# Kernel optimization log

Hardware: AMD Instinct MI355X
Metric: run time of the kernel (lower is better)

Reference implementation:

```python
import jax, jax.numpy as jnp
import numpy as np

D = 1024      # embedding_dim
H = 16        # n_heads
HD = D // H   # head_dim
EPS = 1e-05


def layernorm(x, scale, bias):
    # torch.var default is unbiased (ddof=1) in the original module
    mean = jnp.mean(x, axis=-1, keepdims=True)
    var = jnp.var(x, axis=-1, keepdims=True, ddof=1)
    return scale * (x - mean) / jnp.sqrt(var + EPS) + bias


def gelu(x):
    return 0.5 * x * (1 + jnp.tanh(0.79788456 * (x + 0.044715 * x ** 3)))


def setup_inputs() -> dict:
    key = jax.random.key(0)
    ks = jax.random.split(key, 12)
    s = 0.02
    return {
        "x": jax.random.normal(ks[0], (2, 2048, D), dtype=jnp.float32),
        "Wq": jax.random.normal(ks[1], (D, D), dtype=jnp.float32) * s,
        "Wk": jax.random.normal(ks[2], (D, D), dtype=jnp.float32) * s,
        "Wv": jax.random.normal(ks[3], (D, D), dtype=jnp.float32) * s,
        "Wo": jax.random.normal(ks[4], (D, D), dtype=jnp.float32) * s,
        "bo": jnp.zeros((D,), dtype=jnp.float32),
        "W1": jax.random.normal(ks[5], (D, 4 * D), dtype=jnp.float32) * s,
        "b1": jnp.zeros((4 * D,), dtype=jnp.float32),
        "W2": jax.random.normal(ks[6], (4 * D, D), dtype=jnp.float32) * s,
        "b2": jnp.zeros((D,), dtype=jnp.float32),
        "ln1_scale": jnp.ones((D,), dtype=jnp.float32),
        "ln1_bias": jnp.zeros((D,), dtype=jnp.float32),
        "ln2_scale": jnp.ones((D,), dtype=jnp.float32),
        "ln2_bias": jnp.zeros((D,), dtype=jnp.float32),
    }


def reference(x, Wq, Wk, Wv, Wo, bo, W1, b1, W2, b2,
              ln1_scale, ln1_bias, ln2_scale, ln2_bias):
    B, S, _ = x.shape
    # --- attention sub-block (pre-LN) ---
    h = layernorm(x, ln1_scale, ln1_bias)
    q = (h @ Wq).reshape(B, S, H, HD).transpose(0, 2, 1, 3)  # [B,H,S,HD]
    k = (h @ Wk).reshape(B, S, H, HD).transpose(0, 2, 1, 3)
    v = (h @ Wv).reshape(B, S, H, HD).transpose(0, 2, 1, 3)
    scores = jnp.einsum("bhqd,bhkd->bhqk", q, k)             # [B,H,S,S]
    causal = jnp.tril(jnp.ones((S, S), dtype=bool))
    scores = jnp.where(causal, scores, -jnp.inf)
    attn = jax.nn.softmax(scores / jnp.sqrt(jnp.float32(HD)), axis=-1)
    ctx = jnp.einsum("bhqk,bhkd->bhqd", attn, v)
    ctx = ctx.transpose(0, 2, 1, 3).reshape(B, S, H * HD)
    x = x + (ctx @ Wo + bo)
    # --- FFN sub-block (pre-LN) ---
    h = layernorm(x, ln2_scale, ln2_bias)
    x = x + (gelu(h @ W1 + b1) @ W2 + b2)
    return x
```

## Files before the change

### kernel.cpp

```cpp
#include <hip/hip_runtime.h>
#include <hip/hip_bf16.h>
#include <cstdint>

#define D_DIM 1024
#define S_DIM 2048
#define B_DIM 2
#define NROWS 4096
#define H_DIM 16
#define LOG2E 1.4426950408889634f
#define QSCALE (0.125f * LOG2E)

typedef __bf16 bf16x8 __attribute__((ext_vector_type(8)));
typedef float f32x4 __attribute__((ext_vector_type(4)));
typedef unsigned short u16x8 __attribute__((ext_vector_type(8)));

#define MFMA16(a, b, c) __builtin_amdgcn_mfma_f32_16x16x32_bf16(a, b, c, 0, 0, 0)
#define WBAR __builtin_amdgcn_s_barrier()
#define SB0 __builtin_amdgcn_sched_barrier(0)
#define LGKM0 { asm volatile("s_waitcnt lgkmcnt(0)" ::: "memory"); SB0; }
#define VMW(n) asm volatile("s_waitcnt vmcnt(" #n ")" ::: "memory")

__device__ __forceinline__ void async_cp16(const void* g, void* lds) {
  __builtin_amdgcn_global_load_lds(
      (const __attribute__((address_space(1))) void*)(uintptr_t)g,
      (__attribute__((address_space(3))) void*)(uint32_t)(uintptr_t)lds, 16, 0, 0);
}

__device__ __forceinline__ unsigned short f2bf(float f) {
  __hip_bfloat16 h = __float2bfloat16(f);
  return __builtin_bit_cast(unsigned short, h);
}

__device__ __forceinline__ float bf2f(unsigned short u) {
  return __builtin_bit_cast(float, (unsigned int)u << 16);
}

__device__ __forceinline__ float gelu_fast(float v) {
  float u = v * v;
  float w = v * fmaf(u, 0.044715f, 1.f);
  float e = exp2f(w * -2.3022161f);
  return v * __builtin_amdgcn_rcpf(1.f + e);
}

struct TcArgs {
  const float* src[6];
  __hip_bfloat16* dst[6];
  int K[6];
  int N[6];
  int start[6];
};

__global__ __launch_bounds__(256) void transpose_cast6_kernel(TcArgs a) {
  __shared__ float tile[32][33];
  int bid = blockIdx.x, mi = 0;
#pragma unroll
  for (int i = 1; i < 6; i++)
    if (bid >= a.start[i]) mi = i;
  const float* W = a.src[mi];
  __hip_bfloat16* Wt = a.dst[mi];
  int K = a.K[mi], N = a.N[mi];
  int rel = bid - a.start[mi];
  int tilesx = N >> 5;
  int shift = (N == 4096) ? 7 : 5;
  int n0 = (rel & (tilesx - 1)) * 32, k0 = (rel >> shift) * 32;
  int tx = threadIdx.x, ty = threadIdx.y;
#pragma unroll
  for (int i = 0; i < 32; i += 8)
    tile[ty + i][tx] = W[(size_t)(k0 + ty + i) * N + n0 + tx];
  __syncthreads();
#pragma unroll
  for (int i = 0; i < 32; i += 8)
    Wt[(size_t)(n0 + ty + i) * K + k0 + tx] = __float2bfloat16(tile[tx][ty + i]);
}

__global__ __launch_bounds__(256) void ln_kernel(
    const float* __restrict__ x, const float* __restrict__ sc,
    const float* __restrict__ bi, __hip_bfloat16* __restrict__ out) {
  int row = blockIdx.x, t = threadIdx.x;
  float4 v = ((const float4*)(x + (size_t)row * D_DIM))[t];
  float s = v.x + v.y + v.z + v.w;
  float ss = v.x * v.x + v.y * v.y + v.z * v.z + v.w * v.w;
#pragma unroll
  for (int off = 32; off > 0; off >>= 1) {
    s += __shfl_xor(s, off);
    ss += __shfl_xor(ss, off);
  }
  __shared__ float red[8];
  int wid = t >> 6;
  if ((t & 63) == 0) { red[wid] = s; red[4 + wid] = ss; }
  __syncthreads();
  s = red[0] + red[1] + red[2] + red[3];
  ss = red[4] + red[5] + red[6] + red[7];
  float mean = s * (1.f / 1024.f);
  float var = (ss - 1024.f * mean * mean) * (1.f / 1023.f);
  float inv = rsqrtf(var + 1e-5f);
  float4 scv = ((const float4*)sc)[t];
  float4 biv = ((const float4*)bi)[t];
  ushort4 o;
  o.x = f2bf(scv.x * (v.x - mean) * inv + biv.x);
  o.y = f2bf(scv.y * (v.y - mean) * inv + biv.y);
  o.z = f2bf(scv.z * (v.z - mean) * inv + biv.z);
  o.w = f2bf(scv.w * (v.w - mean) * inv + biv.w);
  ((ushort4*)(out + (size_t)row * D_DIM))[t] = o;
}

template <int EPI>
__global__ __launch_bounds__(256) void gemm128_kernel(
    const __hip_bfloat16* __restrict__ A, const __hip_bfloat16* __restrict__ Bt,
    void* __restrict__ Cout, const float* __restrict__ bias,
    const float* __restrict__ resid, __hip_bfloat16* __restrict__ qb,
    __hip_bfloat16* __restrict__ kb, unsigned short* __restrict__ vt,
    int strideA, int strideB) {
  __shared__ char lds[65536];
  const int t = threadIdx.x;
  const int lane = t & 63, wid = t >> 6;
  const int ql = lane & 15, g = lane >> 4;
  const int wr = wid >> 1, wc = wid & 1;

  const int nbm = gridDim.x, nby = gridDim.y;
  const int lin = blockIdx.y * nbm + blockIdx.x;
  const int q8 = (nbm * nby) >> 3;
  const int u = (lin & 7) * q8 + (lin >> 3);
  const int gi = u >> 5, wi = u & 31;
  const int gpc = nbm >> 2;
  const int gcol = gi / gpc, grow = gi % gpc;
  const int m0 = (grow * 4 + (wi >> 3)) * 128;
  const int n0 = (gcol * 8 + (wi & 7)) * 128;
  const int koff = blockIdx.z * 1024;
  const int sw = (ql & 7) << 4;

  const int srow = t >> 3;
  const int sc16 = (((t & 7) ^ (srow & 7)) << 4);
  const __hip_bfloat16* aB = A + (size_t)(m0 + srow) * strideA + koff + (sc16 >> 1);
  const __hip_bfloat16* bB = Bt + (size_t)(n0 + srow) * strideB + koff + (sc16 >> 1);
  const uint32_t ldsT = (uint32_t)(t * 16);

  auto stg4 = [&](int kt, int s) {
#pragma unroll
    for (int p = 0; p < 4; p++)
      async_cp16(aB + (size_t)(p * 32) * strideA + kt * 64,
                 lds + s * 16384 + p * 4096 + ldsT);
#pragma unroll
    for (int p = 0; p < 4; p++)
      async_cp16(bB + (size_t)(p * 32) * strideB + kt * 64,
                 lds + 32768 + s * 16384 + p * 4096 + ldsT);
  };

  bf16x8 aR[4][2], bR[4][2];
  f32x4 acc[4][4] = {};

  auto ldA = [&](int s) {
    const char* base = lds + s * 16384 + (wr * 64 + ql) * 128;
#pragma unroll
    for (int mi = 0; mi < 4; mi++)
#pragma unroll
      for (int kk = 0; kk < 2; kk++)
        aR[mi][kk] = *(const bf16x8*)(base + mi * 2048 + ((kk * 64 + g * 16) ^ sw));
  };
  auto ldB = [&](int s, int nh) {
    const char* base = lds + 32768 + s * 16384 + (wc * 64 + ql) * 128;
#pragma unroll
    for (int ni = 0; ni < 2; ni++)
#pragma unroll
      for (int kk = 0; kk < 2; kk++)
        bR[nh * 2 + ni][kk] =
            *(const bf16x8*)(base + (nh * 2 + ni) * 2048 + ((kk * 64 + g * 16) ^ sw));
  };
  auto mma = [&](int nh) {
    __builtin_amdgcn_s_setprio(1);
#pragma unroll
    for (int mi = 0; mi < 4; mi++)
#pragma unroll
      for (int ni = 0; ni < 2; ni++) {
        f32x4 c = acc[mi][nh * 2 + ni];
        c = MFMA16(aR[mi][0], bR[nh * 2 + ni][0], c);
        c = MFMA16(aR[mi][1], bR[nh * 2 + ni][1], c);
        acc[mi][nh * 2 + ni] = c;
      }
    __builtin_amdgcn_s_setprio(0);
  };

  stg4(0, 0); stg4(1, 1);
  VMW(8); WBAR;

#pragma unroll 1
  for (int kt = 0; kt < 14; ++kt) {
    const int s = kt & 1;
    ldA(s); ldB(s, 0);
    LGKM0; mma(0);
    ldB(s, 1);
    LGKM0; WBAR; SB0;
    stg4(kt + 2, s);
    mma(1);
    VMW(8); WBAR;
  }
  ldA(0); ldB(0, 0);
  LGKM0; mma(0);
  ldB(0, 1);
  LGKM0; WBAR;
  mma(1);
  VMW(0); WBAR;
  ldA(1); ldB(1, 0);
  LGKM0; mma(0);
  ldB(1, 1);
  LGKM0; mma(1);

#pragma unroll
  for (int mi = 0; mi < 4; mi++) {
    const int row0 = m0 + wr * 64 + mi * 16 + g * 4;
#pragma unroll
    for (int ni = 0; ni < 4; ni++) {
      const int colt = wc * 64 + ni * 16 + ql;
      const f32x4 c = acc[mi][ni];
      if (EPI == 0) {
        const int seg = n0 >> 10;
        const int c1k = (n0 & 1023) + colt;
        if (seg < 2) {
          __hip_bfloat16* Ob = seg == 0 ? qb : kb;
          const float sc = seg == 0 ? QSCALE : 1.f;
#pragma unroll
          for (int rr = 0; rr < 4; rr++)
            Ob[(size_t)(row0 + rr) * 1024 + c1k] = __float2bfloat16(c[rr] * sc);
        } else {
          const int h = c1k >> 6, dh = c1k & 63;
          const int bb = row0 >> 11, s0 = row0 & 2047;
          ushort4 pk;
          pk.x = f2bf(c[0]); pk.y = f2bf(c[1]); pk.z = f2bf(c[2]); pk.w = f2bf(c[3]);
          *(ushort4*)(vt + (((size_t)(bb * 16 + h) * 64 + dh) << 11) + s0) = pk;
        }
      } else if (EPI == 1) {
        const int col = n0 + colt;
        const float bv = bias[col];
#pragma unroll
        for (int rr = 0; rr < 4; rr++)
          ((__hip_bfloat16*)Cout)[(size_t)(row0 + rr) * 4096 + col] =
              __float2bfloat16(gelu_fast(c[rr] + bv));
      } else if (EPI == 2) {
        unsigned short* Cp = (unsigned short*)Cout + (size_t)blockIdx.z * NROWS * 1024;
        const int col = n0 + colt;
#pragma unroll
        for (int rr = 0; rr < 4; rr++)
          Cp[(size_t)(row0 + rr) * 1024 + col] = f2bf(c[rr]);
      } else {
        const int col = n0 + colt;
        const float bv = bias[col];
#pragma unroll
        for (int rr = 0; rr < 4; rr++)
          ((float*)Cout)[(size_t)(row0 + rr) * 1024 + col] =
              c[rr] + bv + resid[(size_t)(row0 + rr) * 1024 + col];
      }
    }
  }
}

__global__ __launch_bounds__(256) void ffn2_reduce_kernel(
    const unsigned short* __restrict__ parts, const float* __restrict__ bias,
    const float* __restrict__ resid, float* __restrict__ out) {
  const size_t i = ((size_t)blockIdx.x * 256 + threadIdx.x) * 8;
  const int col = (int)(i & 1023);
  float a[8];
  float4 r0 = *(const float4*)(resid + i);
  float4 r1 = *(const float4*)(resid + i + 4);
  float4 b0 = *(const float4*)(bias + col);
  float4 b1 = *(const float4*)(bias + col + 4);
  a[0] = r0.x + b0.x; a[1] = r0.y + b0.y; a[2] = r0.z + b0.z; a[3] = r0.w + b0.w;
  a[4] = r1.x + b1.x; a[5] = r1.y + b1.y; a[6] = r1.z + b1.z; a[7] = r1.w + b1.w;
#pragma unroll
  for (int c = 0; c < 4; c++) {
    u16x8 p = *(const u16x8*)(parts + (size_t)c * ((size_t)NROWS * 1024) + i);
#pragma unroll
    for (int j = 0; j < 8; j++) a[j] += bf2f(p[j]);
  }
  float4 o0 = {a[0], a[1], a[2], a[3]};
  float4 o1 = {a[4], a[5], a[6], a[7]};
  *(float4*)(out + i) = o0;
  *(float4*)(out + i + 4) = o1;
}

__global__ __launch_bounds__(256) void attn_kernel(
    const __hip_bfloat16* __restrict__ Q, const __hip_bfloat16* __restrict__ Kb,
    const __hip_bfloat16* __restrict__ Vt, __hip_bfloat16* __restrict__ ctx) {
  __shared__ unsigned short Ks[2][64 * 64];
  __shared__ unsigned short Vs[2][64 * 64];
  __shared__ alignas(16) unsigned short Ps[4][16 * 64];
  const int t = threadIdx.x;
  const int lane = t & 63, wid = t >> 6;
  const int ql = lane & 15, g = lane >> 4;
  const int bid = blockIdx.x;
  const int r4 = bid >> 8, k8 = (bid >> 5) & 7, bh = bid & 31;
  const int qt = (r4 == 0) ? 31 - k8 : (r4 == 1) ? 16 + k8 : (r4 == 2) ? 15 - k8 : k8;
  const int b = bh >> 4, hh = bh & 15;
  const int wq0 = qt * 64 + wid * 16;
  const __hip_bfloat16* qp = Q + (size_t)b * S_DIM * D_DIM + hh * 64;
  const __hip_bfloat16* kp = Kb + (size_t)b * S_DIM * D_DIM + hh * 64;
  const __hip_bfloat16* vp = Vt + (size_t)bh * 64 * S_DIM;
  const int kvend = qt * 64 + 64;
  const int swz = (ql & 7) << 4;
  const f32x4 z4 = {0.f, 0.f, 0.f, 0.f};

  auto stageKV = [&](int buf, int kv0) {
    const int sub = lane >> 3, c = lane & 7;
#pragma unroll
    for (int i = 0; i < 2; i++) {
      const int row = wid * 16 + i * 8 + sub;
      const int cs = (c ^ (row & 7)) * 8;
      async_cp16(kp + (size_t)(kv0 + row) * D_DIM + cs,
                 (char*)&Ks[buf][0] + (wid * 16 + i * 8) * 128);
      async_cp16(vp + (size_t)row * S_DIM + kv0 + cs,
                 (char*)&Vs[buf][0] + (wid * 16 + i * 8) * 128);
    }
  };

  bf16x8 qf[2];
#pragma unroll
  for (int hf = 0; hf < 2; hf++)
    qf[hf] = *(const bf16x8*)(qp + (size_t)(wq0 + ql) * D_DIM + hf * 32 + g * 8);

  float m = -3.0e38f, lsum = 0.f;
  f32x4 acc[4] = {};
  unsigned short* Pw = Ps[wid];

  stageKV(0, 0);
  __syncthreads();
  int cur = 0;
  for (int kv0 = 0; kv0 < kvend; kv0 += 64) {
    if (kv0 + 64 < kvend) stageKV(cur ^ 1, kv0 + 64);

    if (kv0 <= wq0 + 15) {
      const char* Kt = (const char*)&Ks[cur][0];
      f32x4 st[4];
#pragma unroll
      for (int ks = 0; ks < 4; ks++) {
        bf16x8 k0 = *(const bf16x8*)(Kt + (ks * 16 + ql) * 128 + ((g * 16) ^ swz));
        bf16x8 k1 = *(const bf16x8*)(Kt + (ks * 16 + ql) * 128 + (((4 + g) * 16) ^ swz));
        st[ks] = MFMA16(k1, qf[1], MFMA16(k0, qf[0], z4));
      }
      if (kv0 + 63 > wq0) {
#pragma unroll
        for (int ks = 0; ks < 4; ks++)
#pragma unroll
          for (int r = 0; r < 4; r++)
            if (kv0 + ks * 16 + 4 * g + r > wq0 + ql) st[ks][r] = -3.0e38f;
      }
      float tm = -3.0e38f;
#pragma unroll
      for (int ks = 0; ks < 4; ks++)
#pragma unroll
        for (int r = 0; r < 4; r++) tm = fmaxf(tm, st[ks][r]);
      tm = fmaxf(tm, __shfl_xor(tm, 16));
      tm = fmaxf(tm, __shfl_xor(tm, 32));
      if (!__all(tm <= m + 8.f)) {
        const float mn = fmaxf(m, tm);
        const float alpha = exp2f(m - mn);
        lsum *= alpha;
#pragma unroll
        for (int db = 0; db < 4; db++) acc[db] *= alpha;
        m = mn;
      }
      float psum = 0.f;
#pragma unroll
      for (int ks = 0; ks < 4; ks++) {
        float p0 = exp2f(st[ks][0] - m), p1 = exp2f(st[ks][1] - m);
        float p2 = exp2f(st[ks][2] - m), p3 = exp2f(st[ks][3] - m);
        psum += (p0 + p1) + (p2 + p3);
        ushort4 pk;
        pk.x = f2bf(p0); pk.y = f2bf(p1); pk.z = f2bf(p2); pk.w = f2bf(p3);
        *(ushort4*)((char*)Pw + ql * 128 + ((ks * 32 + 8 * g) ^ swz)) = pk;
      }
      psum += __shfl_xor(psum, 16);
      psum += __shfl_xor(psum, 32);
      lsum += psum;

      const char* Vtl = (const char*)&Vs[cur][0];
#pragma unroll
      for (int ksl = 0; ksl < 2; ksl++) {
        bf16x8 pb = *(const bf16x8*)((const char*)Pw + ql * 128 + ((ksl * 64 + 16 * g) ^ swz));
#pragma unroll
        for (int db = 0; db < 4; db++) {
          bf16x8 va = *(const bf16x8*)(Vtl + (db * 16 + ql) * 128 + (((ksl * 4 + g) * 16) ^ swz));
          acc[db] = MFMA16(va, pb, acc[db]);
        }
      }
    }
    __syncthreads();
    cur ^= 1;
  }

  const float inv = 1.f / lsum;
  unsigned short* cp = (unsigned short*)ctx + (size_t)(b * S_DIM + wq0 + ql) * D_DIM + hh * 64;
#pragma unroll
  for (int db = 0; db < 4; db++)
#pragma unroll
    for (int i = 0; i < 2; i++) {
      unsigned int lo = f2bf(acc[db][2 * i] * inv);
      unsigned int hi = f2bf(acc[db][2 * i + 1] * inv);
      *(unsigned int*)(cp + db * 16 + 4 * g + 2 * i) = lo | (hi << 16);
    }
}

extern "C" void kernel_launch(void* const* d_in, const int* in_sizes, int n_in,
                              void* d_out, int out_size, void* d_ws, size_t ws_size,
                              hipStream_t stream) {
  const float* x = (const float*)d_in[0];
  const float* Wq = (const float*)d_in[1];
  const float* Wk = (const float*)d_in[2];
  const float* Wv = (const float*)d_in[3];
  const float* Wo = (const float*)d_in[4];
  const float* bo = (const float*)d_in[5];
  const float* W1 = (const float*)d_in[6];
  const float* b1 = (const float*)d_in[7];
  const float* W2 = (const float*)d_in[8];
  const float* b2 = (const float*)d_in[9];
  const float* ln1s = (const float*)d_in[10];
  const float* ln1b = (const float*)d_in[11];
  const float* ln2s = (const float*)d_in[12];
  const float* ln2b = (const float*)d_in[13];
  float* out = (float*)d_out;

  char* p = (char*)d_ws;
  auto take = [&](size_t n) { char* r = p; p += (n + 255) & ~(size_t)255; return r; };
  __hip_bfloat16* Wqt = (__hip_bfloat16*)take((size_t)1024 * 1024 * 2);
  __hip_bfloat16* Wkt = (__hip_bfloat16*)take((size_t)1024 * 1024 * 2);
  __hip_bfloat16* Wvt = (__hip_bfloat16*)take((size_t)1024 * 1024 * 2);
  __hip_bfloat16* Wot = (__hip_bfloat16*)take((size_t)1024 * 1024 * 2);
  __hip_bfloat16* W1t = (__hip_bfloat16*)take((size_t)4096 * 1024 * 2);
  __hip_bfloat16* W2t = (__hip_bfloat16*)take((size_t)4096 * 1024 * 2);
  __hip_bfloat16* hbuf = (__hip_bfloat16*)take((size_t)NROWS * 1024 * 2);
  __hip_bfloat16* qbuf = (__hip_bfloat16*)take((size_t)NROWS * 1024 * 2);
  __hip_bfloat16* kbuf = (__hip_bfloat16*)take((size_t)NROWS * 1024 * 2);
  __hip_bfloat16* vtbuf = (__hip_bfloat16*)take((size_t)NROWS * 1024 * 2);
  __hip_bfloat16* ctxbuf = (__hip_bfloat16*)take((size_t)NROWS * 1024 * 2);
  float* x1buf = (float*)take((size_t)NROWS * 1024 * 4);
  __hip_bfloat16* h2buf = (__hip_bfloat16*)take((size_t)NROWS * 1024 * 2);
  __hip_bfloat16* gbuf = (__hip_bfloat16*)take((size_t)NROWS * 4096 * 2);
  unsigned short* parts = (unsigned short*)hbuf;

  TcArgs ta;
  ta.src[0] = Wq;  ta.dst[0] = Wqt;  ta.K[0] = 1024; ta.N[0] = 1024; ta.start[0] = 0;
  ta.src[1] = Wk;  ta.dst[1] = Wkt;  ta.K[1] = 1024; ta.N[1] = 1024; ta.start[1] = 1024;
  ta.src[2] = Wv;  ta.dst[2] = Wvt;  ta.K[2] = 1024; ta.N[2] = 1024; ta.start[2] = 2048;
  ta.src[3] = Wo;  ta.dst[3] = Wot;  ta.K[3] = 1024; ta.N[3] = 1024; ta.start[3] = 3072;
  ta.src[4] = W1;  ta.dst[4] = W1t;  ta.K[4] = 1024; ta.N[4] = 4096; ta.start[4] = 4096;
  ta.src[5] = W2;  ta.dst[5] = W2t;  ta.K[5] = 4096; ta.N[5] = 1024; ta.start[5] = 8192;
  transpose_cast6_kernel<<<12288, dim3(32, 8), 0, stream>>>(ta);

  ln_kernel<<<NROWS, 256, 0, stream>>>(x, ln1s, ln1b, hbuf);

  gemm128_kernel<0><<<dim3(32, 24), 256, 0, stream>>>(
      hbuf, Wqt, nullptr, nullptr, nullptr, qbuf, kbuf, (unsigned short*)vtbuf,
      1024, 1024);

  attn_kernel<<<1024, 256, 0, stream>>>(qbuf, kbuf, vtbuf, ctxbuf);

  gemm128_kernel<3><<<dim3(32, 8), 256, 0, stream>>>(
      ctxbuf, Wot, x1buf, bo, x, nullptr, nullptr, nullptr, 1024, 1024);

  ln_kernel<<<NROWS, 256, 0, stream>>>(x1buf, ln2s, ln2b, h2buf);

  gemm128_kernel<1><<<dim3(32, 32), 256, 0, stream>>>(
      h2buf, W1t, gbuf, b1, nullptr, nullptr, nullptr, nullptr, 1024, 1024);

  gemm128_kernel<2><<<dim3(32, 8, 4), 256, 0, stream>>>(
      gbuf, W2t, parts, nullptr, nullptr, nullptr, nullptr, nullptr, 4096, 4096);

  ffn2_reduce_kernel<<<2048, 256, 0, stream>>>(parts, b2, x1buf, out);
}
```

Baseline: 204.8 us.

## Use 256x256-tile double-buffered GEMM for QKV and FFN1 projections

Adds a new 512-thread GEMM kernel with 256x256 output tiles and a simple two-buffer async LDS pipeline. It replaces the 128x128 hand-scheduled kernel for the QKV and FFN1 GEMMs, each wave now computing a 128x64 sub-tile. The larger tiles raise arithmetic intensity per LDS load. In exchange, grids become much smaller (192 and 256 blocks), which risks underfilling the CUs, and the pipeline is simpler, with full barriers in place of the fine-grained waitcnt scheduling. The old epilogue branches are moved into the new kernel.

```diff
diff --git a/kernel.cpp b/kernel.cpp
--- a/kernel.cpp
+++ b/kernel.cpp
@@ -15,10 +15,6 @@
 typedef unsigned short u16x8 __attribute__((ext_vector_type(8)));
 
 #define MFMA16(a, b, c) __builtin_amdgcn_mfma_f32_16x16x32_bf16(a, b, c, 0, 0, 0)
-#define WBAR __builtin_amdgcn_s_barrier()
-#define SB0 __builtin_amdgcn_sched_barrier(0)
-#define LGKM0 { asm volatile("s_waitcnt lgkmcnt(0)" ::: "memory"); SB0; }
-#define VMW(n) asm volatile("s_waitcnt vmcnt(" #n ")" ::: "memory")
 
 __device__ __forceinline__ void async_cp16(const void* g, void* lds) {
   __builtin_amdgcn_global_load_lds(
@@ -105,18 +101,127 @@
 }
 
 template <int EPI>
+__global__ __launch_bounds__(512) void gemm256_2ph_kernel(
+    const __hip_bfloat16* __restrict__ A, const __hip_bfloat16* __restrict__ Bt,
+    void* __restrict__ Cout, const float* __restrict__ bias,
+    __hip_bfloat16* __restrict__ qb, __hip_bfloat16* __restrict__ kb,
+    unsigned short* __restrict__ vt, int strideA, int strideB) {
+  __shared__ __hip_bfloat16 As[2][256 * 64];
+  __shared__ __hip_bfloat16 Bs[2][256 * 64];
+  const int t = threadIdx.x;
+  const int lane = t & 63, wid = t >> 6;
+  const int ql = lane & 15, g = lane >> 4;
+  const int wr = wid >> 2, wc = wid & 3;
+  const int nbx = gridDim.x;
+  const int nwg = nbx * gridDim.y;
+  const int lin = blockIdx.y * nbx + blockIdx.x;
+  const int cpx = nwg >> 3;
+  const int u = (lin & 7) * cpx + (lin >> 3);
+  const int m0 = (u % nbx) * 256, n0 = (u / nbx) * 256;
+  const int sw = (ql & 7) << 4;
+
+  const int srow = t >> 3;
+  const int sc16 = (((t & 7) ^ (srow & 7)) << 4);
+  const __hip_bfloat16* aB = A + (size_t)(m0 + srow) * strideA + (sc16 >> 1);
+  const __hip_bfloat16* bB = Bt + (size_t)(n0 + srow) * strideB + (sc16 >> 1);
+  const uint32_t ldsT = (uint32_t)(t * 16);
+
+  auto stage = [&](int buf, int kt) {
+#pragma unroll
+    for (int p = 0; p < 4; p++)
+      async_cp16(aB + (size_t)(p * 64) * strideA + kt * 64,
+                 (char*)&As[buf][0] + p * 8192 + ldsT);
+#pragma unroll
+    for (int p = 0; p < 4; p++)
+      async_cp16(bB + (size_t)(p * 64) * strideB + kt * 64,
+                 (char*)&Bs[buf][0] + p * 8192 + ldsT);
+  };
+
+  f32x4 acc[8][4] = {};
+
+  auto compute = [&](int buf) {
+    bf16x8 bR[4][2];
+    const char* bbase = (const char*)&Bs[buf][0] + (wc * 64 + ql) * 128;
+#pragma unroll
+    for (int ni = 0; ni < 4; ni++)
+#pragma unroll
+      for (int kk = 0; kk < 2; kk++)
+        bR[ni][kk] = *(const bf16x8*)(bbase + ni * 2048 + ((kk * 64 + g * 16) ^ sw));
+    const char* abase = (const char*)&As[buf][0] + (wr * 128 + ql) * 128;
+#pragma unroll
+    for (int mi = 0; mi < 8; mi++) {
+      bf16x8 a0 = *(const bf16x8*)(abase + mi * 2048 + ((g * 16) ^ sw));
+      bf16x8 a1 = *(const bf16x8*)(abase + mi * 2048 + ((64 + g * 16) ^ sw));
+#pragma unroll
+      for (int ni = 0; ni < 4; ni++) {
+        f32x4 c = acc[mi][ni];
+        c = MFMA16(a0, bR[ni][0], c);
+        c = MFMA16(a1, bR[ni][1], c);
+        acc[mi][ni] = c;
+      }
+    }
+  };
+
+  stage(0, 0);
+  __syncthreads();
+  int cur = 0;
+  for (int kt = 0; kt < 15; ++kt) {
+    stage(cur ^ 1, kt + 1);
+    compute(cur);
+    __syncthreads();
+    cur ^= 1;
+  }
+  compute(cur);
+
+#pragma unroll
+  for (int mi = 0; mi < 8; mi++) {
+    const int row0 = m0 + wr * 128 + mi * 16 + (g << 2);
+#pragma unroll
+    for (int ni = 0; ni < 4; ni++) {
+      const int col = n0 + wc * 64 + ni * 16 + ql;
+      const f32x4 c = acc[mi][ni];
+      if (EPI == 0) {
+        const int seg = col >> 10;
+        const int c1k = col & 1023;
+        if (seg < 2) {
+          __hip_bfloat16* Ob = seg == 0 ? qb : kb;
+          const float sc = seg == 0 ? QSCALE : 1.f;
+#pragma unroll
+          for (int rr = 0; rr < 4; rr++)
+            Ob[(size_t)(row0 + rr) * 1024 + c1k] = __float2bfloat16(c[rr] * sc);
+        } else {
+          const int h = c1k >> 6, dh = c1k & 63;
+          const int bb = row0 >> 11, s0 = row0 & 2047;
+          ushort4 pk;
+          pk.x = f2bf(c[0]); pk.y = f2bf(c[1]); pk.z = f2bf(c[2]); pk.w = f2bf(c[3]);
+          *(ushort4*)(vt + (((size_t)(bb * 16 + h) * 64 + dh) << 11) + s0) = pk;
+        }
+      } else {
+        const float bv = bias[col];
+#pragma unroll
+        for (int rr = 0; rr < 4; rr++)
+          ((__hip_bfloat16*)Cout)[(size_t)(row0 + rr) * 4096 + col] =
+              __float2bfloat16(gelu_fast(c[rr] + bv));
+      }
+    }
+  }
+}
+
+#define WBAR __builtin_amdgcn_s_barrier()
+#define SB0 __builtin_amdgcn_sched_barrier(0)
+#define LGKM0 { asm volatile("s_waitcnt lgkmcnt(0)" ::: "memory"); SB0; }
+#define VMW(n) asm volatile("s_waitcnt vmcnt(" #n ")" ::: "memory")
+
+template <int EPI>
 __global__ __launch_bounds__(256) void gemm128_kernel(
     const __hip_bfloat16* __restrict__ A, const __hip_bfloat16* __restrict__ Bt,
     void* __restrict__ Cout, const float* __restrict__ bias,
-    const float* __restrict__ resid, __hip_bfloat16* __restrict__ qb,
-    __hip_bfloat16* __restrict__ kb, unsigned short* __restrict__ vt,
-    int strideA, int strideB) {
+    const float* __restrict__ resid, int strideA, int strideB) {
   __shared__ char lds[65536];
   const int t = threadIdx.x;
   const int lane = t & 63, wid = t >> 6;
   const int ql = lane & 15, g = lane >> 4;
   const int wr = wid >> 1, wc = wid & 1;
-
   const int nbm = gridDim.x, nby = gridDim.y;
   const int lin = blockIdx.y * nbm + blockIdx.x;
   const int q8 = (nbm * nby) >> 3;
@@ -207,42 +312,17 @@
 
 #pragma unroll
   for (int mi = 0; mi < 4; mi++) {
-    const int row0 = m0 + wr * 64 + mi * 16 + g * 4;
+    const int row0 = m0 + wr * 64 + mi * 16 + (g << 2);
 #pragma unroll
     for (int ni = 0; ni < 4; ni++) {
-      const int colt = wc * 64 + ni * 16 + ql;
+      const int col = n0 + wc * 64 + ni * 16 + ql;
       const f32x4 c = acc[mi][ni];
-      if (EPI == 0) {
-        const int seg = n0 >> 10;
-        const int c1k = (n0 & 1023) + colt;
-        if (seg < 2) {
-          __hip_bfloat16* Ob = seg == 0 ? qb : kb;
-          const float sc = seg == 0 ? QSCALE : 1.f;
-#pragma unroll
-          for (int rr = 0; rr < 4; rr++)
-            Ob[(size_t)(row0 + rr) * 1024 + c1k] = __float2bfloat16(c[rr] * sc);
-        } else {
-          const int h = c1k >> 6, dh = c1k & 63;
-          const int bb = row0 >> 11, s0 = row0 & 2047;
-          ushort4 pk;
-          pk.x = f2bf(c[0]); pk.y = f2bf(c[1]); pk.z = f2bf(c[2]); pk.w = f2bf(c[3]);
-          *(ushort4*)(vt + (((size_t)(bb * 16 + h) * 64 + dh) << 11) + s0) = pk;
-        }
-      } else if (EPI == 1) {
-        const int col = n0 + colt;
-        const float bv = bias[col];
-#pragma unroll
-        for (int rr = 0; rr < 4; rr++)
-          ((__hip_bfloat16*)Cout)[(size_t)(row0 + rr) * 4096 + col] =
-              __float2bfloat16(gelu_fast(c[rr] + bv));
-      } else if (EPI == 2) {
+      if (EPI == 2) {
         unsigned short* Cp = (unsigned short*)Cout + (size_t)blockIdx.z * NROWS * 1024;
-        const int col = n0 + colt;
 #pragma unroll
         for (int rr = 0; rr < 4; rr++)
           Cp[(size_t)(row0 + rr) * 1024 + col] = f2bf(c[rr]);
       } else {
-        const int col = n0 + colt;
         const float bv = bias[col];
 #pragma unroll
         for (int rr = 0; rr < 4; rr++)
@@ -446,22 +526,21 @@
 
   ln_kernel<<<NROWS, 256, 0, stream>>>(x, ln1s, ln1b, hbuf);
 
-  gemm128_kernel<0><<<dim3(32, 24), 256, 0, stream>>>(
-      hbuf, Wqt, nullptr, nullptr, nullptr, qbuf, kbuf, (unsigned short*)vtbuf,
-      1024, 1024);
+  gemm256_2ph_kernel<0><<<dim3(16, 12), 512, 0, stream>>>(
+      hbuf, Wqt, nullptr, nullptr, qbuf, kbuf, (unsigned short*)vtbuf, 1024, 1024);
 
   attn_kernel<<<1024, 256, 0, stream>>>(qbuf, kbuf, vtbuf, ctxbuf);
 
   gemm128_kernel<3><<<dim3(32, 8), 256, 0, stream>>>(
-      ctxbuf, Wot, x1buf, bo, x, nullptr, nullptr, nullptr, 1024, 1024);
+      ctxbuf, Wot, x1buf, bo, x, 1024, 1024);
 
   ln_kernel<<<NROWS, 256, 0, stream>>>(x1buf, ln2s, ln2b, h2buf);
 
-  gemm128_kernel<1><<<dim3(32, 32), 256, 0, stream>>>(
-      h2buf, W1t, gbuf, b1, nullptr, nullptr, nullptr, nullptr, 1024, 1024);
+  gemm256_2ph_kernel<1><<<dim3(16, 16), 512, 0, stream>>>(
+      h2buf, W1t, gbuf, b1, nullptr, nullptr, nullptr, 1024, 1024);
 
   gemm128_kernel<2><<<dim3(32, 8, 4), 256, 0, stream>>>(
-      gbuf, W2t, parts, nullptr, nullptr, nullptr, nullptr, nullptr, 4096, 4096);
+      gbuf, W2t, parts, nullptr, nullptr, 4096, 4096);
 
   ffn2_reduce_kernel<<<2048, 256, 0, stream>>>(parts, b2, x1buf, out);
 }
```

After: 205.8 us. Within noise of the previous version (+0.5%).
